# Performance work log

Hardware: AMD Instinct MI355X
Metric: run time of the kernel (lower is better)

## Reference

```python
import jax, jax.numpy as jnp
import numpy as np

NUM_CLASSES = 80
REG_MAX = 16
PI = 3.141592653589793
B, L = 8, 21504


def _cross2(a, b):
    return a[..., 0] * b[..., 1] - a[..., 1] * b[..., 0]


def _box2corners(box):  # (N,5) xywh+angle -> (N,4,2)
    x, y, w, h, a = (box[:, i] for i in range(5))
    tx = jnp.asarray([0.5, -0.5, -0.5, 0.5], box.dtype)
    ty = jnp.asarray([0.5, 0.5, -0.5, -0.5], box.dtype)
    cx = tx[None, :] * w[:, None]
    cy = ty[None, :] * h[:, None]
    c, s = jnp.cos(a)[:, None], jnp.sin(a)[:, None]
    rx = cx * c - cy * s
    ry = cx * s + cy * c
    return jnp.stack([rx + x[:, None], ry + y[:, None]], axis=-1)


def _edge_intersections(c1, c2):
    # all 4x4 edge-pair segment intersections
    p = c1[:, :, None, :]                           # (N,4,1,2)
    q = jnp.roll(c1, -1, axis=1)[:, :, None, :]
    r = c2[:, None, :, :]                           # (N,1,4,2)
    s = jnp.roll(c2, -1, axis=1)[:, None, :, :]
    d1, d2, rp = q - p, s - r, r - p
    den = _cross2(d1, d2)                           # (N,4,4)
    safe = jnp.where(jnp.abs(den) < 1e-12, 1.0, den)
    t = _cross2(rp, d2) / safe
    u = _cross2(rp, d1) / safe
    valid = (jnp.abs(den) > 1e-12) & (t > 0) & (t < 1) & (u > 0) & (u < 1)
    pts = p + t[..., None] * d1                     # (N,4,4,2)
    return pts, valid


def _corners_in_box(corners, ref):
    # project onto two adjacent edges of the reference box
    a, b, d = ref[:, 0:1], ref[:, 1:2], ref[:, 3:4]  # (N,1,2)
    ab, ad, ap = b - a, d - a, corners - a
    pab = (ap * ab).sum(-1) / jnp.maximum((ab * ab).sum(-1), 1e-12)
    pad = (ap * ad).sum(-1) / jnp.maximum((ad * ad).sum(-1), 1e-12)
    e = 1e-6
    return (pab > -e) & (pab < 1 + e) & (pad > -e) & (pad < 1 + e)


def _convex_area(vertices, mask):  # (N,24,2),(N,24) -> (N,)
    nv = mask.sum(-1)
    mf = mask.astype(vertices.dtype)[..., None]
    mean = (vertices * mf).sum(1) / jnp.maximum(nv, 1).astype(vertices.dtype)[:, None]
    cen = (vertices - mean[:, None, :]) * mf        # invalid -> 0 after centering
    ang = jnp.where(mask, jnp.arctan2(cen[..., 1], cen[..., 0]), 1e9)
    order = jnp.argsort(ang, axis=1)                # valid vertices CCW, invalid last
    sv = jnp.take_along_axis(cen, order[..., None], axis=1)
    x, y = sv[..., 0], sv[..., 1]
    crosses = (x[:, :-1] * y[:, 1:] - x[:, 1:] * y[:, :-1]).sum(-1)
    last = jnp.clip(nv - 1, 0, 23)
    vlast = jnp.take_along_axis(sv, jnp.broadcast_to(last[:, None, None], (sv.shape[0], 1, 2)), axis=1)[:, 0]
    v0 = sv[:, 0]
    closing = vlast[:, 0] * v0[:, 1] - v0[:, 0] * vlast[:, 1]
    return 0.5 * jnp.abs(crosses + closing)


def _diff_iou_rotated_2d(b1, b2):  # (N,5) each -> (N,)
    c1, c2 = _box2corners(b1), _box2corners(b2)
    n = b1.shape[0]
    pts, pmask = _edge_intersections(c1, c2)
    m1 = _corners_in_box(c1, c2)
    m2 = _corners_in_box(c2, c1)
    verts = jnp.concatenate([c1, c2, pts.reshape(n, 16, 2)], axis=1)   # (N,24,2)
    mask = jnp.concatenate([m1, m2, pmask.reshape(n, 16)], axis=1)
    inter = _convex_area(verts, mask)
    a1 = b1[:, 2] * b1[:, 3]
    a2 = b2[:, 2] * b2[:, 3]
    return inter / (a1 + a2 - inter + 1e-8)


def _bbox2dist(anchor_points, bbox, reg_max):
    x1y1, x2y2 = bbox[..., :2], bbox[..., 2:]
    return jnp.clip(jnp.concatenate([anchor_points - x1y1, x2y2 - anchor_points], -1), 0.0, reg_max - 0.01)


def _forward(pred_dist, pred_bboxes, pred_angles, anchor_points,
             target_bboxes, target_angles, target_scores, target_scores_sum, fg_mask):
    b, l = fg_mask.shape
    n = b * l
    fgf = fg_mask.astype(pred_bboxes.dtype)
    pa = pred_angles / 180.0 * PI
    ta = target_angles / 180.0 * PI
    pred_r = jnp.concatenate([pred_bboxes, pa], -1).reshape(n, 5)
    targ_r = jnp.concatenate([target_bboxes, ta], -1).reshape(n, 5)
    ious = jnp.clip(_diff_iou_rotated_2d(pred_r, targ_r).reshape(b, l), 1e-6, None)
    iou_loss = 1.0 - ious  # linear mode
    bbox_weight = target_scores.sum(-1)  # (B,L)
    tss = target_scores_sum.reshape(())
    denom = jnp.where(tss == 0, 1.0, tss)
    loss_iou = (iou_loss * bbox_weight * fgf).sum() / denom
    # DFL term
    target_ltrb = _bbox2dist(anchor_points, target_bboxes, REG_MAX)  # (B,L,4)
    tl = jnp.clip(target_ltrb.astype(jnp.int32), 0, REG_MAX - 1)
    wl = (tl + 1).astype(target_ltrb.dtype) - target_ltrb
    wr = 1.0 - wl
    logp = jax.nn.log_softmax(pred_dist.reshape(b, l, 4, REG_MAX + 1), axis=-1)
    ll = -jnp.take_along_axis(logp, tl[..., None], axis=-1)[..., 0] * wl
    lr = -jnp.take_along_axis(logp, (tl + 1)[..., None], axis=-1)[..., 0] * wr
    dfl = (ll + lr).mean(-1)  # (B,L)
    loss_dfl = (dfl * bbox_weight * fgf).sum() / denom
    return loss_iou, loss_dfl


def setup_inputs() -> dict:
    key = jax.random.key(0)
    ks = jax.random.split(key, 10)

    def boxes(k):
        kxy, kwh = jax.random.split(k)
        xy = jax.random.uniform(kxy, (B, L, 2)) * 640.0
        wh = jax.random.uniform(kwh, (B, L, 2)) * 96.0 + 4.0
        return jnp.concatenate([xy, wh], -1).astype(jnp.float32)

    pred_bboxes = boxes(ks[0])
    target_bboxes = boxes(ks[1])
    pred_angles = (jax.random.uniform(ks[2], (B, L, 1)) * 180.0).astype(jnp.float32)
    target_angles = (jax.random.uniform(ks[3], (B, L, 1)) * 180.0).astype(jnp.float32)
    pred_dist = jax.random.normal(ks[4], (B, L, 4 * (REG_MAX + 1)), dtype=jnp.float32)
    anchor_points = (jax.random.uniform(ks[5], (L, 2)) * 640.0).astype(jnp.float32)
    target_scores = (jax.random.uniform(ks[6], (B, L, NUM_CLASSES)) * 0.1).astype(jnp.float32)
    fg_mask = jax.random.uniform(ks[7], (B, L)) < 0.1
    target_scores_sum = jnp.maximum(target_scores.sum(), 1.0).reshape(1)
    return {
        'pred_dist': pred_dist,
        'pred_bboxes': pred_bboxes,
        'pred_angles': pred_angles,
        'anchor_points': anchor_points,
        'target_bboxes': target_bboxes,
        'target_angles': target_angles,
        'target_scores': target_scores,
        'target_scores_sum': target_scores_sum,
        'fg_mask': fg_mask,
    }


def reference(pred_dist, pred_bboxes, pred_angles, anchor_points,
              target_bboxes, target_angles, target_scores, target_scores_sum, fg_mask):
    return _forward(pred_dist, pred_bboxes, pred_angles, anchor_points,
                    target_bboxes, target_angles, target_scores, target_scores_sum, fg_mask)
```

## Files before the change

kernel.cpp:

```cpp
#include <hip/hip_runtime.h>
#include <math.h>

#define NCLS 80
#define LL 21504
#define NNELEM 172032
#define EPB 128
#define NB 1344

template <bool STRICT>
__device__ __forceinline__ float clip_piece(float Ax, float Ay, float Bx, float By,
                                            const float (&nx)[4], const float (&ny)[4],
                                            const float (&off)[4]) {
  const float Dx = Bx - Ax, Dy = By - Ay;
  float t0 = 0.f, t1 = 1.f;
  bool rej = false;
#pragma unroll
  for (int k = 0; k < 4; ++k) {
    const float den = nx[k] * Dx + ny[k] * Dy;
    const float num = nx[k] * Ax + ny[k] * Ay - off[k];
    const float tt = -num / den;
    if (den > 0.f)      t0 = fmaxf(t0, tt);
    else if (den < 0.f) t1 = fminf(t1, tt);
    else                rej = rej || (STRICT ? (num <= 0.f) : (num < 0.f));
  }
  const float X0 = fmaf(t0, Dx, Ax), Y0 = fmaf(t0, Dy, Ay);
  const float X1 = fmaf(t1, Dx, Ax), Y1 = fmaf(t1, Dy, Ay);
  return (!rej && (t0 < t1)) ? (X0 * Y1 - X1 * Y0) : 0.f;
}

__device__ __forceinline__ void heavy_elem(
    int idx,
    const float* __restrict__ pred_dist,
    const float* __restrict__ pred_bboxes,
    const float* __restrict__ pred_angles,
    const float* __restrict__ anchor_points,
    const float* __restrict__ target_bboxes,
    const float* __restrict__ target_angles,
    const float* __restrict__ target_scores,
    float& ci, float& cd) {
  const int l = idx % LL;
  const float4 pb = ((const float4*)pred_bboxes)[idx];
  const float4 tb = ((const float4*)target_bboxes)[idx];
  const float kD2R = 0.017453292519943295f;
  float sp, cp, st, ct;
  __sincosf(pred_angles[idx] * kD2R, &sp, &cp);
  __sincosf(target_angles[idx] * kD2R, &st, &ct);

  const float tx[4] = {0.5f, -0.5f, -0.5f, 0.5f};
  const float ty[4] = {0.5f, 0.5f, -0.5f, -0.5f};
  const float qcx = tb.x - pb.x, qcy = tb.y - pb.y;
  float pxx[4], pyy[4], qxx[4], qyy[4];
#pragma unroll
  for (int k = 0; k < 4; ++k) {
    float lx = tx[k] * pb.z, ly = ty[k] * pb.w;
    pxx[k] = lx * cp - ly * sp;
    pyy[k] = lx * sp + ly * cp;
    lx = tx[k] * tb.z; ly = ty[k] * tb.w;
    qxx[k] = lx * ct - ly * st + qcx;
    qyy[k] = lx * st + ly * ct + qcy;
  }
  float pnx[4], pny[4], pof[4], qnx[4], qny[4], qof[4];
#pragma unroll
  for (int k = 0; k < 4; ++k) {
    const int kp = (k + 1) & 3;
    pnx[k] = pyy[k] - pyy[kp]; pny[k] = pxx[kp] - pxx[k];
    pof[k] = pnx[k] * pxx[k] + pny[k] * pyy[k];
    qnx[k] = qyy[k] - qyy[kp]; qny[k] = qxx[kp] - qxx[k];
    qof[k] = qnx[k] * qxx[k] + qny[k] * qyy[k];
  }
  float s2 = 0.f;
#pragma unroll
  for (int i = 0; i < 4; ++i) {
    const int ip = (i + 1) & 3;
    s2 += clip_piece<false>(pxx[i], pyy[i], pxx[ip], pyy[ip], qnx, qny, qof);
  }
#pragma unroll
  for (int i = 0; i < 4; ++i) {
    const int ip = (i + 1) & 3;
    s2 += clip_piece<true>(qxx[i], qyy[i], qxx[ip], qyy[ip], pnx, pny, pof);
  }
  const float inter = 0.5f * fabsf(s2);
  const float a1 = pb.z * pb.w, a2 = tb.z * tb.w;
  const float iou = fmaxf(inter / (a1 + a2 - inter + 1e-8f), 1e-6f);
  const float iou_loss = 1.f - iou;

  const float4* sp4 = (const float4*)(target_scores + (size_t)idx * NCLS);
  float bw = 0.f;
#pragma unroll
  for (int k = 0; k < NCLS / 4; ++k) {
    const float4 v = sp4[k];
    bw += (v.x + v.y) + (v.z + v.w);
  }

  const float2 anc = ((const float2*)anchor_points)[l];
  float dists[4];
  dists[0] = fminf(fmaxf(anc.x - tb.x, 0.f), 15.99f);
  dists[1] = fminf(fmaxf(anc.y - tb.y, 0.f), 15.99f);
  dists[2] = fminf(fmaxf(tb.z - anc.x, 0.f), 15.99f);
  dists[3] = fminf(fmaxf(tb.w - anc.y, 0.f), 15.99f);
  const float* dr = pred_dist + (size_t)idx * 68;
  float4 v4[17];
#pragma unroll
  for (int k = 0; k < 17; ++k) v4[k] = ((const float4*)dr)[k];
  float vv[68];
#pragma unroll
  for (int k = 0; k < 17; ++k) {
    vv[4 * k] = v4[k].x; vv[4 * k + 1] = v4[k].y;
    vv[4 * k + 2] = v4[k].z; vv[4 * k + 3] = v4[k].w;
  }
  const float kLog2e = 1.4426950408889634f;
  const float kLn2 = 0.6931471805599453f;
  float dfl = 0.f;
#pragma unroll
  for (int s = 0; s < 4; ++s) {
    float mx = vv[17 * s];
#pragma unroll
    for (int k = 1; k < 17; ++k) mx = fmaxf(mx, vv[17 * s + k]);
    float se = 0.f;
#pragma unroll
    for (int k = 0; k < 17; ++k) se += exp2f((vv[17 * s + k] - mx) * kLog2e);
    const float lz = mx + log2f(se) * kLn2;
    const float t = dists[s];
    int tl = (int)t;
    tl = tl < 0 ? 0 : (tl > 15 ? 15 : tl);
    const float wl = (float)(tl + 1) - t;
    const float wr = 1.f - wl;
    const float* row = dr + s * 17;
    dfl -= (row[tl] - lz) * wl + (row[tl + 1] - lz) * wr;
  }
  dfl *= 0.25f;

  ci = fmaf(iou_loss, bw, ci);
  cd = fmaf(dfl, bw, cd);
}

__global__ __launch_bounds__(64) void main_kernel(
    const float* __restrict__ pred_dist,
    const float* __restrict__ pred_bboxes,
    const float* __restrict__ pred_angles,
    const float* __restrict__ anchor_points,
    const float* __restrict__ target_bboxes,
    const float* __restrict__ target_angles,
    const float* __restrict__ target_scores,
    const void* __restrict__ fgp,
    float2* __restrict__ partials) {
  const int blk = blockIdx.x;
  const int lane = threadIdx.x;
  const int base = blk * EPB;

  unsigned int x = ((const unsigned int*)fgp)[lane];
#pragma unroll
  for (int o = 32; o >= 1; o >>= 1) x |= __shfl_xor(x, o);
  const bool isByte = ((x & ~0x01010101u) == 0u) && (x > 1u);

  unsigned int bits;
  if (isByte) {
    const unsigned short v = ((const unsigned short*)fgp)[blk * 64 + lane];
    bits = ((v & 0xFFu) ? 1u : 0u) | ((v >> 8) ? 2u : 0u);
  } else {
    const uint2 w = ((const uint2*)fgp)[blk * 64 + lane];
    bits = (w.x ? 1u : 0u) | (w.y ? 2u : 0u);
  }

  const int cnt = __popc(bits);
  int pre = cnt;
#pragma unroll
  for (int o = 1; o < 64; o <<= 1) {
    const int v = __shfl_up(pre, o);
    if (lane >= o) pre += v;
  }
  const int total = __shfl(pre, 63);
  int wo = pre - cnt;
  __shared__ unsigned short sl[EPB];
  if (bits & 1u) { sl[wo] = (unsigned short)(lane * 2); ++wo; }
  if (bits & 2u) { sl[wo] = (unsigned short)(lane * 2 + 1); }

  float ci = 0.f, cd = 0.f;
  for (int j = lane; j < total; j += 64) {
    heavy_elem(base + (int)sl[j], pred_dist, pred_bboxes, pred_angles,
               anchor_points, target_bboxes, target_angles, target_scores,
               ci, cd);
  }
#pragma unroll
  for (int o = 32; o >= 1; o >>= 1) {
    ci += __shfl_xor(ci, o);
    cd += __shfl_xor(cd, o);
  }
  if (lane == 0) partials[blk] = make_float2(ci, cd);
}

__global__ __launch_bounds__(512) void final_kernel(
    const float2* __restrict__ partials,
    const float* __restrict__ tss_p,
    float* __restrict__ out) {
  const int t = threadIdx.x;
  float a = 0.f, b = 0.f;
#pragma unroll
  for (int i = 0; i < 3; ++i) {
    const int j = t + i * 512;
    if (j < NB) { const float2 p = partials[j]; a += p.x; b += p.y; }
  }
#pragma unroll
  for (int o = 32; o >= 1; o >>= 1) {
    a += __shfl_xor(a, o);
    b += __shfl_xor(b, o);
  }
  __shared__ float sa[8], sb[8];
  const int w = t >> 6;
  if ((t & 63) == 0) { sa[w] = a; sb[w] = b; }
  __syncthreads();
  if (t == 0) {
    float s0 = 0.f, s1 = 0.f;
#pragma unroll
    for (int i = 0; i < 8; ++i) { s0 += sa[i]; s1 += sb[i]; }
    const float ts = tss_p[0];
    const float denom = (ts == 0.f) ? 1.f : ts;
    out[0] = s0 / denom;
    out[1] = s1 / denom;
  }
}

extern "C" void kernel_launch(void* const* d_in, const int* in_sizes, int n_in,
                              void* d_out, int out_size, void* d_ws, size_t ws_size,
                              hipStream_t stream) {
  const float* pred_dist      = (const float*)d_in[0];
  const float* pred_bboxes    = (const float*)d_in[1];
  const float* pred_angles    = (const float*)d_in[2];
  const float* anchor_points  = (const float*)d_in[3];
  const float* target_bboxes  = (const float*)d_in[4];
  const float* target_angles  = (const float*)d_in[5];
  const float* target_scores  = (const float*)d_in[6];
  const float* tss            = (const float*)d_in[7];
  const void*  fgp            = d_in[8];

  float2* partials = (float2*)d_ws;
  float* out = (float*)d_out;

  main_kernel<<<NB, 64, 0, stream>>>(pred_dist, pred_bboxes, pred_angles,
                                     anchor_points, target_bboxes, target_angles,
                                     target_scores, fgp, partials);
  final_kernel<<<1, 512, 0, stream>>>(partials, tss, out);
}
```

Measured before the change: 18.61 us.

## Process each foreground element with a 4-lane team instead of one thread

Each selected element is now handled by four lanes. Each lane takes one clip edge pair, one quarter of the class-score sum and one of the four DFL sides, and the partial results are combined with xor shuffles. This spreads the per-element work over more lanes, which should cut the per-thread register footprint (the 68-float array) and shorten the critical path, since only about 13 foreground elements exist per 128-element block. In exchange, the box corners are computed redundantly in all four lanes, shuffle and select overhead is added, and the block's elements are now covered in more loop passes of 16 teams.

```diff
diff --git a/kernel.cpp b/kernel.cpp
--- a/kernel.cpp
+++ b/kernel.cpp
@@ -28,8 +28,15 @@
   return (!rej && (t0 < t1)) ? (X0 * Y1 - X1 * Y0) : 0.f;
 }
 
-__device__ __forceinline__ void heavy_elem(
-    int idx,
+__device__ __forceinline__ float sel4(float a0, float a1, float a2, float a3, int i) {
+  float r = (i == 1) ? a1 : a0;
+  r = (i == 2) ? a2 : r;
+  r = (i == 3) ? a3 : r;
+  return r;
+}
+
+__device__ __forceinline__ void team_elem(
+    int idx, int sub,
     const float* __restrict__ pred_dist,
     const float* __restrict__ pred_bboxes,
     const float* __restrict__ pred_angles,
@@ -68,70 +75,72 @@
     qnx[k] = qyy[k] - qyy[kp]; qny[k] = qxx[kp] - qxx[k];
     qof[k] = qnx[k] * qxx[k] + qny[k] * qyy[k];
   }
-  float s2 = 0.f;
-#pragma unroll
-  for (int i = 0; i < 4; ++i) {
-    const int ip = (i + 1) & 3;
-    s2 += clip_piece<false>(pxx[i], pyy[i], pxx[ip], pyy[ip], qnx, qny, qof);
-  }
-#pragma unroll
-  for (int i = 0; i < 4; ++i) {
-    const int ip = (i + 1) & 3;
-    s2 += clip_piece<true>(qxx[i], qyy[i], qxx[ip], qyy[ip], pnx, pny, pof);
-  }
+
+  const int subp = (sub + 1) & 3;
+  const float pax = sel4(pxx[0], pxx[1], pxx[2], pxx[3], sub);
+  const float pay = sel4(pyy[0], pyy[1], pyy[2], pyy[3], sub);
+  const float pbx = sel4(pxx[0], pxx[1], pxx[2], pxx[3], subp);
+  const float pby = sel4(pyy[0], pyy[1], pyy[2], pyy[3], subp);
+  const float qax = sel4(qxx[0], qxx[1], qxx[2], qxx[3], sub);
+  const float qay = sel4(qyy[0], qyy[1], qyy[2], qyy[3], sub);
+  const float qbx = sel4(qxx[0], qxx[1], qxx[2], qxx[3], subp);
+  const float qby = sel4(qyy[0], qyy[1], qyy[2], qyy[3], subp);
+  float s2 = clip_piece<false>(pax, pay, pbx, pby, qnx, qny, qof) +
+             clip_piece<true>(qax, qay, qbx, qby, pnx, pny, pof);
+  s2 += __shfl_xor(s2, 1);
+  s2 += __shfl_xor(s2, 2);
+
   const float inter = 0.5f * fabsf(s2);
   const float a1 = pb.z * pb.w, a2 = tb.z * tb.w;
   const float iou = fmaxf(inter / (a1 + a2 - inter + 1e-8f), 1e-6f);
   const float iou_loss = 1.f - iou;
 
-  const float4* sp4 = (const float4*)(target_scores + (size_t)idx * NCLS);
+  const float4* sp4 = (const float4*)(target_scores + (size_t)idx * NCLS) + sub * 5;
   float bw = 0.f;
 #pragma unroll
-  for (int k = 0; k < NCLS / 4; ++k) {
+  for (int k = 0; k < 5; ++k) {
     const float4 v = sp4[k];
     bw += (v.x + v.y) + (v.z + v.w);
   }
+  bw += __shfl_xor(bw, 1);
+  bw += __shfl_xor(bw, 2);
 
   const float2 anc = ((const float2*)anchor_points)[l];
-  float dists[4];
-  dists[0] = fminf(fmaxf(anc.x - tb.x, 0.f), 15.99f);
-  dists[1] = fminf(fmaxf(anc.y - tb.y, 0.f), 15.99f);
-  dists[2] = fminf(fmaxf(tb.z - anc.x, 0.f), 15.99f);
-  dists[3] = fminf(fmaxf(tb.w - anc.y, 0.f), 15.99f);
-  const float* dr = pred_dist + (size_t)idx * 68;
-  float4 v4[17];
-#pragma unroll
-  for (int k = 0; k < 17; ++k) v4[k] = ((const float4*)dr)[k];
-  float vv[68];
-#pragma unroll
-  for (int k = 0; k < 17; ++k) {
-    vv[4 * k] = v4[k].x; vv[4 * k + 1] = v4[k].y;
-    vv[4 * k + 2] = v4[k].z; vv[4 * k + 3] = v4[k].w;
-  }
+  const float d0 = anc.x - tb.x, d1 = anc.y - tb.y;
+  const float d2 = tb.z - anc.x, d3 = tb.w - anc.y;
+  const float t = fminf(fmaxf(sel4(d0, d1, d2, d3, sub), 0.f), 15.99f);
+  const float* row = pred_dist + (size_t)idx * 68 + sub * 17;
+  float vv[17];
+#pragma unroll
+  for (int k = 0; k < 17; ++k) vv[k] = row[k];
+  float mx = vv[0];
+#pragma unroll
+  for (int k = 1; k < 17; ++k) mx = fmaxf(mx, vv[k]);
   const float kLog2e = 1.4426950408889634f;
   const float kLn2 = 0.6931471805599453f;
-  float dfl = 0.f;
-#pragma unroll
-  for (int s = 0; s < 4; ++s) {
-    float mx = vv[17 * s];
-#pragma unroll
-    for (int k = 1; k < 17; ++k) mx = fmaxf(mx, vv[17 * s + k]);
-    float se = 0.f;
-#pragma unroll
-    for (int k = 0; k < 17; ++k) se += exp2f((vv[17 * s + k] - mx) * kLog2e);
-    const float lz = mx + log2f(se) * kLn2;
-    const float t = dists[s];
-    int tl = (int)t;
-    tl = tl < 0 ? 0 : (tl > 15 ? 15 : tl);
-    const float wl = (float)(tl + 1) - t;
-    const float wr = 1.f - wl;
-    const float* row = dr + s * 17;
-    dfl -= (row[tl] - lz) * wl + (row[tl + 1] - lz) * wr;
-  }
+  float se = 0.f;
+#pragma unroll
+  for (int k = 0; k < 17; ++k) se += exp2f((vv[k] - mx) * kLog2e);
+  const float lz = mx + log2f(se) * kLn2;
+  int tl = (int)t;
+  tl = tl < 0 ? 0 : (tl > 15 ? 15 : tl);
+  const float wl = (float)(tl + 1) - t;
+  const float wr = 1.f - wl;
+  float vtl = vv[0], vtl1 = vv[1];
+#pragma unroll
+  for (int k = 1; k < 16; ++k) {
+    vtl  = (k == tl) ? vv[k]     : vtl;
+    vtl1 = (k == tl) ? vv[k + 1] : vtl1;
+  }
+  float dfl = -((vtl - lz) * wl + (vtl1 - lz) * wr);
+  dfl += __shfl_xor(dfl, 1);
+  dfl += __shfl_xor(dfl, 2);
   dfl *= 0.25f;
 
-  ci = fmaf(iou_loss, bw, ci);
-  cd = fmaf(dfl, bw, cd);
+  if (sub == 0) {
+    ci = fmaf(iou_loss, bw, ci);
+    cd = fmaf(dfl, bw, cd);
+  }
 }
 
 __global__ __launch_bounds__(64) void main_kernel(
@@ -175,11 +184,12 @@
   if (bits & 1u) { sl[wo] = (unsigned short)(lane * 2); ++wo; }
   if (bits & 2u) { sl[wo] = (unsigned short)(lane * 2 + 1); }
 
+  const int team = lane >> 2, sub = lane & 3;
   float ci = 0.f, cd = 0.f;
-  for (int j = lane; j < total; j += 64) {
-    heavy_elem(base + (int)sl[j], pred_dist, pred_bboxes, pred_angles,
-               anchor_points, target_bboxes, target_angles, target_scores,
-               ci, cd);
+  for (int j = team; j < total; j += 16) {
+    team_elem(base + (int)sl[j], sub, pred_dist, pred_bboxes, pred_angles,
+              anchor_points, target_bboxes, target_angles, target_scores,
+              ci, cd);
   }
 #pragma unroll
   for (int o = 32; o >= 1; o >>= 1) {
```

Measured after the change: 15.86 us. 1.17x faster.
